# Performance work log

Hardware: AMD Instinct MI355X
Metric: run time of the kernel (lower is better)

Reference implementation:

```python
import jax, jax.numpy as jnp
import numpy as np

B, S, D, H, FF, P = 16, 200, 512, 8, 2048, 10
HD = D // H
EPS = 1e-5


def _pe2d(h, w, ch):
    # Faithful numpy port of PositionalEncoding2D (positional_encodings lib)
    channels = int(np.ceil(ch / 4) * 2)
    inv_freq = 1.0 / (10000.0 ** (np.arange(0, channels, 2, dtype=np.float32) / channels))
    sin_x = np.einsum('i,j->ij', np.arange(h, dtype=np.float32), inv_freq)
    sin_y = np.einsum('i,j->ij', np.arange(w, dtype=np.float32), inv_freq)
    emb_x = np.stack([np.sin(sin_x), np.cos(sin_x)], -1).reshape(h, channels)
    emb_y = np.stack([np.sin(sin_y), np.cos(sin_y)], -1).reshape(w, channels)
    emb = np.zeros((h, w, 2 * channels), dtype=np.float32)
    emb[:, :, :channels] = emb_x[:, None, :]
    emb[:, :, channels:2 * channels] = emb_y[None, :, :]
    return emb[:, :, :ch]


def _xavier(key, shape):
    fan_out, fan_in = shape
    lim = float(np.sqrt(6.0 / (fan_in + fan_out)))
    return jax.random.uniform(key, shape, minval=-lim, maxval=lim, dtype=jnp.float32)


def setup_inputs():
    key = jax.random.key(0)
    ks = jax.random.split(key, 8)
    x = jax.random.normal(ks[0], (B, S, D), dtype=jnp.float32)
    pos = jnp.asarray(_pe2d(S, S, P))  # (S, S, P) positional bias features
    Wkv = _xavier(ks[1], (2 * D, D)); bkv = jnp.zeros((2 * D,))
    Wo = _xavier(ks[2], (D, D)); bo = jnp.zeros((D,))
    Wpos = _xavier(ks[3], (1, P)); bpos = jnp.zeros((1,))
    W1 = _xavier(ks[4], (FF, D)); b1 = jnp.zeros((FF,))
    W2 = _xavier(ks[5], (D, FF)); b2 = jnp.zeros((D,))
    g1 = jnp.ones((D,)); beta1 = jnp.zeros((D,))
    g2 = jnp.ones((D,)); beta2 = jnp.zeros((D,))
    return {"x": x, "pos": pos, "Wkv": Wkv, "bkv": bkv, "Wo": Wo, "bo": bo,
            "Wpos": Wpos, "bpos": bpos, "W1": W1, "b1": b1, "W2": W2, "b2": b2,
            "g1": g1, "beta1": beta1, "g2": g2, "beta2": beta2}


def _layernorm(x, g, b):
    mu = jnp.mean(x, axis=-1, keepdims=True)
    var = jnp.mean(jnp.square(x - mu), axis=-1, keepdims=True)
    return (x - mu) * jax.lax.rsqrt(var + EPS) * g + b


def reference(x, pos, Wkv, bkv, Wo, bo, Wpos, bpos, W1, b1, W2, b2, g1, beta1, g2, beta2):
    # --- MultiheadAttention_KV (attn_type='kv') ---
    kv = x @ Wkv.T + bkv                                   # (B,S,2D)
    kv = kv.reshape(B, S, H, 2 * HD).transpose(0, 2, 1, 3)  # (B,H,S,2hd)
    k, v = kv[..., :HD], kv[..., HD:]
    attn = jnp.einsum('bhid,bhjd->bhij', k, k) / jnp.sqrt(jnp.float32(HD))
    # map_pos is linear: map_pos(attn[...,None] + pos) == attn*sum(w) + (pos@w + b)
    # -> same math as materializing the (B,H,S,S,P) tensor, but fused.
    pos_bias = pos @ Wpos[0] + bpos[0]                     # (S,S)
    scores = attn * jnp.sum(Wpos) + pos_bias[None, None]
    a = jax.nn.softmax(scores, axis=-1)
    vals = jnp.einsum('bhij,bhjd->bhid', a, v)             # (B,H,S,hd)
    vals = vals.transpose(0, 2, 1, 3).reshape(B, S, D)
    o = vals @ Wo.T + bo
    # --- residual + post-norm ---
    h = _layernorm(x + o, g1, beta1)
    # --- FFN ---
    ff = jax.nn.relu(h @ W1.T + b1) @ W2.T + b2
    return _layernorm(h + ff, g2, beta2)
```

## Files before the change

### kernel.cpp

```cpp
#include <hip/hip_runtime.h>
#include <hip/hip_bf16.h>

#define EPSV 1e-5f
static const int B_ = 16, S_ = 200, D_ = 512, H_ = 8, FF_ = 2048, P_ = 10, HD_ = 64;
static const int SP = 224;

typedef __bf16 bf16_t;
typedef __attribute__((ext_vector_type(8))) __bf16 bf16x8;
typedef __attribute__((ext_vector_type(4))) __bf16 bf16x4;
typedef __attribute__((ext_vector_type(4))) float f32x4;

__device__ __forceinline__ void gload16(const void* g, void* l) {
    __builtin_amdgcn_global_load_lds(
        (const __attribute__((address_space(1))) void*)g,
        (__attribute__((address_space(3))) void*)l, 16, 0, 0);
}

template <int BM, int BN, int WROWS, int WCOLS, int EPI, int NSPLIT, int KC>
__global__ __launch_bounds__(256) void mfma_gemm(
    const bf16_t* __restrict__ A,
    const bf16_t* __restrict__ Bw,
    float* __restrict__ Cf, bf16_t* __restrict__ Cb, long cBat, int ldc,
    const float* __restrict__ bias,
    bf16_t* __restrict__ kOut, bf16_t* __restrict__ vtOut,
    int M, int N, int K)
{
    constexpr int MR = WROWS / 16, NR = WCOLS / 16;
    constexpr int NWC = BN / WCOLS;
    constexpr int NIT = KC / 64;
    static_assert((4 / NWC) * WROWS == BM, "wave tiling must cover BM");
    static_assert(NWC * WCOLS == BN, "wave tiling must cover BN");

    __shared__ bf16_t Asm[2][BM * 64];
    __shared__ bf16_t Bsm[2][BN * 64];

    const int wv = threadIdx.x >> 6;
    const int ln = threadIdx.x & 63;
    const int split = blockIdx.z;
    const int rowBase = blockIdx.y * BM;
    const int colBase = blockIdx.x * BN;
    const int wr = (wv / NWC) * WROWS;
    const int wc = (wv % NWC) * WCOLS;

    const int lr8 = ln >> 3;
    const int lc = (ln & 7) * 8;
    const int kBeg = split * KC;

    f32x4 acc[MR][NR] = {};

    auto STAGE = [&](int k0, int buf) {
        #pragma unroll
        for (int i = 0; i < BM / 32; i++) {
            int row = i * 32 + wv * 8 + lr8;
            int gr = rowBase + row; gr = (gr < M) ? gr : (M - 1);
            gload16(A + (long)gr * K + k0 + lc, &Asm[buf][(i * 32 + wv * 8) * 64]);
        }
        #pragma unroll
        for (int i = 0; i < BN / 32; i++) {
            int col = i * 32 + wv * 8 + lr8;
            int gc = colBase + col; gc = (gc < N) ? gc : (N - 1);
            gload16(Bw + (long)gc * K + k0 + lc, &Bsm[buf][(i * 32 + wv * 8) * 64]);
        }
    };

    auto COMPUTE = [&](int buf) {
        #pragma unroll
        for (int kk = 0; kk < 2; kk++) {
            bf16x8 af[MR], bfr[NR];
            #pragma unroll
            for (int m = 0; m < MR; m++)
                af[m] = *reinterpret_cast<const bf16x8*>(
                    &Asm[buf][(wr + m * 16 + (ln & 15)) * 64 + kk * 32 + (ln >> 4) * 8]);
            #pragma unroll
            for (int n = 0; n < NR; n++)
                bfr[n] = *reinterpret_cast<const bf16x8*>(
                    &Bsm[buf][(wc + n * 16 + (ln & 15)) * 64 + kk * 32 + (ln >> 4) * 8]);
            #pragma unroll
            for (int m = 0; m < MR; m++)
                #pragma unroll
                for (int n = 0; n < NR; n++)
                    acc[m][n] = __builtin_amdgcn_mfma_f32_16x16x32_bf16(
                        af[m], bfr[n], acc[m][n], 0, 0, 0);
        }
    };

    STAGE(kBeg, 0);
    __syncthreads();

    #pragma unroll
    for (int t = 0; t < NIT; t++) {
        if (t + 1 < NIT) STAGE(kBeg + (t + 1) * 64, (t + 1) & 1);
        COMPUTE(t & 1);
        if (t + 1 < NIT) __syncthreads();
    }

    #pragma unroll
    for (int m = 0; m < MR; m++) {
        #pragma unroll
        for (int n = 0; n < NR; n++) {
            #pragma unroll
            for (int r = 0; r < 4; r++) {
                int row = rowBase + wr + m * 16 + (ln >> 4) * 4 + r;
                int col = colBase + wc + n * 16 + (ln & 15);
                if (row >= M || col >= N) continue;
                float v = acc[m][n][r];
                if constexpr (EPI == 3) {
                    v += bias[col];
                    int b = row / S_, s = row - b * S_;
                    int h = col >> 7, w = col & 127;
                    if (w < HD_)
                        kOut[((long)(b * H_ + h) * SP + s) * HD_ + w] = (bf16_t)v;
                    else
                        vtOut[((long)(b * H_ + h) * HD_ + (w - HD_)) * SP + s] = (bf16_t)v;
                } else if constexpr (EPI == 1) {
                    v += bias[col];
                    v = fmaxf(v, 0.f);
                    Cb[(long)row * ldc + col] = (bf16_t)v;
                } else {
                    Cf[(long)split * cBat + (long)row * ldc + col] = v;
                }
            }
        }
    }
}

__global__ __launch_bounds__(256) void attn_fused(
    const bf16_t* __restrict__ Kb, const bf16_t* __restrict__ Vt,
    const float* __restrict__ G, const float* __restrict__ scalePtr,
    bf16_t* __restrict__ vals)
{
    __shared__ __align__(16) bf16_t Pl[4][16][232];

    const int bh = blockIdx.x;
    const int tile = blockIdx.y;
    const int wv = threadIdx.x >> 6;
    const int ln = threadIdx.x & 63;
    const int b = bh >> 3, h = bh & 7;
    const int rowBase = tile * 64 + wv * 16;

    const bf16_t* Kbh = Kb + (long)bh * SP * HD_;
    const bf16_t* Vbh = Vt + (long)bh * HD_ * SP;
    const float scale = scalePtr[0];

    const int lr = ln & 15;
    const int lk = (ln >> 4) * 8;

    f32x4 acc[14];
    #pragma unroll
    for (int n = 0; n < 14; n++) acc[n] = (f32x4){0.f, 0.f, 0.f, 0.f};

    int arow = rowBase + lr; arow = (arow < S_) ? arow : (S_ - 1);
    const bf16x8 a0 = *reinterpret_cast<const bf16x8*>(Kbh + (long)arow * HD_ + lk);
    const bf16x8 a1 = *reinterpret_cast<const bf16x8*>(Kbh + (long)arow * HD_ + 32 + lk);

    #pragma unroll
    for (int n = 0; n < 14; n++) {
        const bf16_t* bp = Kbh + (long)(n * 16 + lr) * HD_;
        bf16x8 b0 = *reinterpret_cast<const bf16x8*>(bp + lk);
        bf16x8 b1 = *reinterpret_cast<const bf16x8*>(bp + 32 + lk);
        acc[n] = __builtin_amdgcn_mfma_f32_16x16x32_bf16(a0, b0, acc[n], 0, 0, 0);
        acc[n] = __builtin_amdgcn_mfma_f32_16x16x32_bf16(a1, b1, acc[n], 0, 0, 0);
    }

    float Gc[14];
    #pragma unroll
    for (int n = 0; n < 14; n++) Gc[n] = G[n * 16 + lr];

    #pragma unroll
    for (int r = 0; r < 4; r++) {
        float m = -1e30f;
        #pragma unroll
        for (int n = 0; n < 14; n++) {
            float v = acc[n][r] * scale + Gc[n];
            acc[n][r] = v;
            m = fmaxf(m, v);
        }
        #pragma unroll
        for (int off = 1; off < 16; off <<= 1) m = fmaxf(m, __shfl_xor(m, off));
        float s = 0.f;
        #pragma unroll
        for (int n = 0; n < 14; n++) {
            float e = __expf(acc[n][r] - m);
            acc[n][r] = e;
            s += e;
        }
        #pragma unroll
        for (int off = 1; off < 16; off <<= 1) s += __shfl_xor(s, off);
        float inv = 1.f / s;
        #pragma unroll
        for (int n = 0; n < 14; n++) acc[n][r] *= inv;
    }

    #pragma unroll
    for (int n = 0; n < 14; n++)
        #pragma unroll
        for (int r = 0; r < 4; r++)
            Pl[wv][(ln >> 4) * 4 + r][n * 16 + lr] = (bf16_t)acc[n][r];

    f32x4 vacc[4] = {};
    #pragma unroll
    for (int kk = 0; kk < 7; kk++) {
        bf16x8 pa = *reinterpret_cast<const bf16x8*>(&Pl[wv][lr][kk * 32 + lk]);
        #pragma unroll
        for (int n = 0; n < 4; n++) {
            bf16x8 vb = *reinterpret_cast<const bf16x8*>(
                Vbh + (long)(n * 16 + lr) * SP + kk * 32 + lk);
            vacc[n] = __builtin_amdgcn_mfma_f32_16x16x32_bf16(pa, vb, vacc[n], 0, 0, 0);
        }
    }

    #pragma unroll
    for (int n = 0; n < 4; n++) {
        #pragma unroll
        for (int r = 0; r < 4; r++) {
            int row = rowBase + (ln >> 4) * 4 + r;
            if (row < S_)
                vals[((long)b * S_ + row) * D_ + h * HD_ + n * 16 + lr] =
                    (bf16_t)vacc[n][r];
        }
    }
}

__global__ __launch_bounds__(256) void prep_all(
    const float* __restrict__ x, const float* __restrict__ Wkv,
    const float* __restrict__ Wo, const float* __restrict__ W1,
    const float* __restrict__ W2, bf16_t* __restrict__ dst,
    float4* __restrict__ zeroP,
    const float* __restrict__ pos, const float* __restrict__ Wpos,
    float* __restrict__ G, float* __restrict__ scal)
{
    const int gid = blockIdx.x * blockDim.x + threadIdx.x;
    const int nthr = gridDim.x * blockDim.x;

    for (int i = gid; i < 1130496; i += nthr) {
        long e = (long)i * 4;
        const float* s; long off;
        if (e < 1638400)      { s = x;   off = e; }
        else if (e < 2162688) { s = Wkv; off = e - 1638400; }
        else if (e < 2424832) { s = Wo;  off = e - 2162688; }
        else if (e < 3473408) { s = W1;  off = e - 2424832; }
        else                  { s = W2;  off = e - 3473408; }
        float4 v = *reinterpret_cast<const float4*>(s + off);
        bf16x4 o = {(bf16_t)v.x, (bf16_t)v.y, (bf16_t)v.z, (bf16_t)v.w};
        *reinterpret_cast<bf16x4*>(dst + e) = o;
    }
    for (int i = gid; i < 458752; i += nthr)
        zeroP[i] = make_float4(0.f, 0.f, 0.f, 0.f);
    if (gid < SP) {
        float g = -1e30f;
        if (gid < S_) {
            g = 0.f;
            #pragma unroll
            for (int p = 6; p < 10; p++) g += pos[(long)gid * P_ + p] * Wpos[p];
        }
        G[gid] = g;
    }
    if (gid == 0) {
        float sw = 0.f;
        for (int p = 0; p < P_; p++) sw += Wpos[p];
        scal[0] = sw * 0.125f;
    }
}

template <int NPART>
__global__ __launch_bounds__(256) void add_ln_p(
    const float* __restrict__ a, const float* __restrict__ parts, long partStride,
    const float* __restrict__ bias,
    const float* __restrict__ g, const float* __restrict__ beta,
    float* __restrict__ outf, bf16_t* __restrict__ outb, int rows)
{
    int row = blockIdx.x * 4 + (threadIdx.x >> 6);
    int lane = threadIdx.x & 63;
    if (row >= rows) return;
    long base = (long)row * D_;
    float v[8];
    float sum = 0.f;
    #pragma unroll
    for (int i = 0; i < 8; i++) {
        int c = lane + i * 64;
        float t = a[base + c] + bias[c];
        #pragma unroll
        for (int p = 0; p < NPART; p++) t += parts[p * partStride + base + c];
        v[i] = t;
        sum += t;
    }
    #pragma unroll
    for (int off = 32; off; off >>= 1) sum += __shfl_xor(sum, off);
    float mean = sum * (1.f / 512.f);
    float var = 0.f;
    #pragma unroll
    for (int i = 0; i < 8; i++) { float d = v[i] - mean; var += d * d; }
    #pragma unroll
    for (int off = 32; off; off >>= 1) var += __shfl_xor(var, off);
    float rstd = rsqrtf(var * (1.f / 512.f) + EPSV);
    #pragma unroll
    for (int i = 0; i < 8; i++) {
        int c = lane + i * 64;
        float o = (v[i] - mean) * rstd * g[c] + beta[c];
        outf[base + c] = o;
        if (outb) outb[base + c] = (bf16_t)o;
    }
}

extern "C" void kernel_launch(void* const* d_in, const int* in_sizes, int n_in,
                              void* d_out, int out_size, void* d_ws, size_t ws_size,
                              hipStream_t stream)
{
    const float* x    = (const float*)d_in[0];
    const float* pos  = (const float*)d_in[1];
    const float* Wkv  = (const float*)d_in[2];
    const float* bkv  = (const float*)d_in[3];
    const float* Wo   = (const float*)d_in[4];
    const float* bo   = (const float*)d_in[5];
    const float* Wpos = (const float*)d_in[6];
    const float* W1   = (const float*)d_in[8];
    const float* b1   = (const float*)d_in[9];
    const float* W2   = (const float*)d_in[10];
    const float* b2   = (const float*)d_in[11];
    const float* g1   = (const float*)d_in[12];
    const float* be1  = (const float*)d_in[13];
    const float* g2   = (const float*)d_in[14];
    const float* be2  = (const float*)d_in[15];
    float* out = (float*)d_out;

    char* w = (char*)d_ws;
    bf16_t* xb   = (bf16_t*)(w + 0);
    bf16_t* Wkvb = (bf16_t*)(w + 3276800);
    bf16_t* Wob  = (bf16_t*)(w + 4325376);
    bf16_t* W1b  = (bf16_t*)(w + 4849664);
    bf16_t* W2b  = (bf16_t*)(w + 6946816);
    bf16_t* Kb   = (bf16_t*)(w + 9043968);
    bf16_t* Vt   = (bf16_t*)(w + 12713984);
    float*  G    = (float*)(w + 16384000);
    float*  scal = (float*)(w + 16384896);
    bf16_t* vals = (bf16_t*)(w + 16385024);
    float*  hf   = (float*)(w + 19661824);
    bf16_t* hb   = (bf16_t*)(w + 26215424);
    float*  obuf = (float*)(w + 29492224);
    bf16_t* tb   = (bf16_t*)(w + 42599424);
    float*  fbuf = (float*)(w + 55706624);

    const int M = B_ * S_;
    const long PS = (long)M * D_;

    prep_all<<<2048, 256, 0, stream>>>(x, Wkv, Wo, W1, W2, xb, (float4*)Kb,
                                       pos, Wpos, G, scal);

    mfma_gemm<64, 64, 32, 32, 3, 1, 512><<<dim3(16, 50, 1), 256, 0, stream>>>(
        xb, Wkvb, nullptr, nullptr, 0, 0, bkv, Kb, Vt, M, 2 * D_, D_);

    attn_fused<<<dim3(128, 4, 1), 256, 0, stream>>>(Kb, Vt, G, scal, vals);

    mfma_gemm<64, 64, 32, 32, 5, 2, 256><<<dim3(8, 50, 2), 256, 0, stream>>>(
        vals, Wob, obuf, nullptr, PS, D_, nullptr, nullptr, nullptr, M, D_, D_);

    add_ln_p<2><<<(M + 3) / 4, 256, 0, stream>>>(x, obuf, PS, bo, g1, be1, hf, hb, M);

    mfma_gemm<64, 64, 32, 32, 1, 1, 512><<<dim3(32, 50, 1), 256, 0, stream>>>(
        hb, W1b, nullptr, tb, 0, FF_, b1, nullptr, nullptr, M, FF_, D_);

    mfma_gemm<64, 64, 32, 32, 5, 4, 512><<<dim3(8, 50, 4), 256, 0, stream>>>(
        tb, W2b, fbuf, nullptr, PS, D_, nullptr, nullptr, nullptr, M, D_, FF_);

    add_ln_p<4><<<(M + 3) / 4, 256, 0, stream>>>(hf, fbuf, PS, b2, g2, be2, out, nullptr, M);
}
```

Before: 118.8 us.

## Use 128x64 GEMM tiles, drop LDS double buffering, halve FFN2 split-K

All GEMMs switch from 64x64 to 128x64 block tiles with 64x32 wave tiles, halving the grid rows. The double-buffered LDS pipeline is replaced with a single buffer, a runtime K loop, and a sync before and after each compute step. The W2 GEMM now splits K two ways instead of four, and the final layernorm sums two partials. This gives more reuse per block and fewer partial sums, but loses global-load/compute overlap and launches fewer blocks.

```diff
diff --git a/kernel.cpp b/kernel.cpp
--- a/kernel.cpp
+++ b/kernel.cpp
@@ -16,23 +16,22 @@
         (__attribute__((address_space(3))) void*)l, 16, 0, 0);
 }
 
-template <int BM, int BN, int WROWS, int WCOLS, int EPI, int NSPLIT, int KC>
+template <int BM, int BN, int WROWS, int WCOLS, int EPI>
 __global__ __launch_bounds__(256) void mfma_gemm(
     const bf16_t* __restrict__ A,
     const bf16_t* __restrict__ Bw,
     float* __restrict__ Cf, bf16_t* __restrict__ Cb, long cBat, int ldc,
     const float* __restrict__ bias,
     bf16_t* __restrict__ kOut, bf16_t* __restrict__ vtOut,
-    int M, int N, int K)
+    int M, int N, int K, int kcPerSplit)
 {
     constexpr int MR = WROWS / 16, NR = WCOLS / 16;
     constexpr int NWC = BN / WCOLS;
-    constexpr int NIT = KC / 64;
     static_assert((4 / NWC) * WROWS == BM, "wave tiling must cover BM");
     static_assert(NWC * WCOLS == BN, "wave tiling must cover BN");
 
-    __shared__ bf16_t Asm[2][BM * 64];
-    __shared__ bf16_t Bsm[2][BN * 64];
+    __shared__ bf16_t Asm[BM * 64];
+    __shared__ bf16_t Bsm[BN * 64];
 
     const int wv = threadIdx.x >> 6;
     const int ln = threadIdx.x & 63;
@@ -44,37 +43,38 @@
 
     const int lr8 = ln >> 3;
     const int lc = (ln & 7) * 8;
-    const int kBeg = split * KC;
 
     f32x4 acc[MR][NR] = {};
 
-    auto STAGE = [&](int k0, int buf) {
+    const int kBeg = split * kcPerSplit;
+    const int kEnd = kBeg + kcPerSplit;
+
+    for (int k0 = kBeg; k0 < kEnd; k0 += 64) {
         #pragma unroll
         for (int i = 0; i < BM / 32; i++) {
             int row = i * 32 + wv * 8 + lr8;
             int gr = rowBase + row; gr = (gr < M) ? gr : (M - 1);
-            gload16(A + (long)gr * K + k0 + lc, &Asm[buf][(i * 32 + wv * 8) * 64]);
+            gload16(A + (long)gr * K + k0 + lc, &Asm[(i * 32 + wv * 8) * 64]);
         }
         #pragma unroll
         for (int i = 0; i < BN / 32; i++) {
             int col = i * 32 + wv * 8 + lr8;
             int gc = colBase + col; gc = (gc < N) ? gc : (N - 1);
-            gload16(Bw + (long)gc * K + k0 + lc, &Bsm[buf][(i * 32 + wv * 8) * 64]);
-        }
-    };
-
-    auto COMPUTE = [&](int buf) {
+            gload16(Bw + (long)gc * K + k0 + lc, &Bsm[(i * 32 + wv * 8) * 64]);
+        }
+        __syncthreads();
+
         #pragma unroll
         for (int kk = 0; kk < 2; kk++) {
             bf16x8 af[MR], bfr[NR];
             #pragma unroll
             for (int m = 0; m < MR; m++)
                 af[m] = *reinterpret_cast<const bf16x8*>(
-                    &Asm[buf][(wr + m * 16 + (ln & 15)) * 64 + kk * 32 + (ln >> 4) * 8]);
+                    &Asm[(wr + m * 16 + (ln & 15)) * 64 + kk * 32 + (ln >> 4) * 8]);
             #pragma unroll
             for (int n = 0; n < NR; n++)
                 bfr[n] = *reinterpret_cast<const bf16x8*>(
-                    &Bsm[buf][(wc + n * 16 + (ln & 15)) * 64 + kk * 32 + (ln >> 4) * 8]);
+                    &Bsm[(wc + n * 16 + (ln & 15)) * 64 + kk * 32 + (ln >> 4) * 8]);
             #pragma unroll
             for (int m = 0; m < MR; m++)
                 #pragma unroll
@@ -82,16 +82,7 @@
                     acc[m][n] = __builtin_amdgcn_mfma_f32_16x16x32_bf16(
                         af[m], bfr[n], acc[m][n], 0, 0, 0);
         }
-    };
-
-    STAGE(kBeg, 0);
-    __syncthreads();
-
-    #pragma unroll
-    for (int t = 0; t < NIT; t++) {
-        if (t + 1 < NIT) STAGE(kBeg + (t + 1) * 64, (t + 1) & 1);
-        COMPUTE(t & 1);
-        if (t + 1 < NIT) __syncthreads();
+        __syncthreads();
     }
 
     #pragma unroll
@@ -346,21 +337,21 @@
     prep_all<<<2048, 256, 0, stream>>>(x, Wkv, Wo, W1, W2, xb, (float4*)Kb,
                                        pos, Wpos, G, scal);
 
-    mfma_gemm<64, 64, 32, 32, 3, 1, 512><<<dim3(16, 50, 1), 256, 0, stream>>>(
-        xb, Wkvb, nullptr, nullptr, 0, 0, bkv, Kb, Vt, M, 2 * D_, D_);
+    mfma_gemm<128, 64, 64, 32, 3><<<dim3(16, 25, 1), 256, 0, stream>>>(
+        xb, Wkvb, nullptr, nullptr, 0, 0, bkv, Kb, Vt, M, 2 * D_, D_, D_);
 
     attn_fused<<<dim3(128, 4, 1), 256, 0, stream>>>(Kb, Vt, G, scal, vals);
 
-    mfma_gemm<64, 64, 32, 32, 5, 2, 256><<<dim3(8, 50, 2), 256, 0, stream>>>(
-        vals, Wob, obuf, nullptr, PS, D_, nullptr, nullptr, nullptr, M, D_, D_);
+    mfma_gemm<128, 64, 64, 32, 5><<<dim3(8, 25, 2), 256, 0, stream>>>(
+        vals, Wob, obuf, nullptr, PS, D_, nullptr, nullptr, nullptr, M, D_, D_, 256);
 
     add_ln_p<2><<<(M + 3) / 4, 256, 0, stream>>>(x, obuf, PS, bo, g1, be1, hf, hb, M);
 
-    mfma_gemm<64, 64, 32, 32, 1, 1, 512><<<dim3(32, 50, 1), 256, 0, stream>>>(
-        hb, W1b, nullptr, tb, 0, FF_, b1, nullptr, nullptr, M, FF_, D_);
-
-    mfma_gemm<64, 64, 32, 32, 5, 4, 512><<<dim3(8, 50, 4), 256, 0, stream>>>(
-        tb, W2b, fbuf, nullptr, PS, D_, nullptr, nullptr, nullptr, M, D_, FF_);
-
-    add_ln_p<4><<<(M + 3) / 4, 256, 0, stream>>>(hf, fbuf, PS, b2, g2, be2, out, nullptr, M);
-}
+    mfma_gemm<128, 64, 64, 32, 1><<<dim3(32, 25, 1), 256, 0, stream>>>(
+        hb, W1b, nullptr, tb, 0, FF_, b1, nullptr, nullptr, M, FF_, D_, D_);
+
+    mfma_gemm<128, 64, 64, 32, 5><<<dim3(8, 25, 2), 256, 0, stream>>>(
+        tb, W2b, fbuf, nullptr, PS, D_, nullptr, nullptr, nullptr, M, D_, FF_, 1024);
+
+    add_ln_p<2><<<(M + 3) / 4, 256, 0, stream>>>(hf, fbuf, PS, b2, g2, be2, out, nullptr, M);
+}
```

Result: faster. 115.0 us (-3.1%).
